# Performance work log

Measured on AMD Instinct MI355X. Metric: run time of the kernel, lower is better.

## Reference

```python
import jax, jax.numpy as jnp
import numpy as np

B, NQ, NKV = 4, 1024, 2048
DQ, DC, DI, H = 1024, 1024, 1024, 16
DH = DI // H
EPS = 1e-5


def layer_norm(x, gamma, beta):
    mu = jnp.mean(x, axis=-1, keepdims=True)
    var = jnp.var(x, axis=-1, keepdims=True)
    return (x - mu) * jax.lax.rsqrt(var + EPS) * gamma + beta


def setup_inputs() -> dict:
    key = jax.random.key(0)
    ks = jax.random.split(key, 6)
    s = 0.02
    return {
        "q": jax.random.normal(ks[0], (B, NQ, DQ), jnp.float32),
        "context": jax.random.normal(ks[1], (B, NKV, DC), jnp.float32),
        "Wq": jax.random.normal(ks[2], (DI, DQ), jnp.float32) * s,
        "Wkv": jax.random.normal(ks[3], (2 * DI, DC), jnp.float32) * s,
        "Wproj": jax.random.normal(ks[4], (DQ, DI), jnp.float32) * s,
        "bproj": jnp.zeros((DQ,), jnp.float32),
        "q_gamma": jnp.ones((DQ,), jnp.float32),
        "q_beta": jnp.zeros((DQ,), jnp.float32),
        "c_gamma": jnp.ones((DC,), jnp.float32),
        "c_beta": jnp.zeros((DC,), jnp.float32),
    }


def reference(q, context, Wq, Wkv, Wproj, bproj, q_gamma, q_beta, c_gamma, c_beta):
    scale = DH ** -0.5
    qn = layer_norm(q, q_gamma, q_beta)            # [b, nq, dq]
    cn = layer_norm(context, c_gamma, c_beta)      # [b, nkv, dc]
    qp = qn @ Wq.T                                  # [b, nq, di]
    kv = cn @ Wkv.T                                 # [b, nkv, 2*di]
    k, v = kv[..., :DI], kv[..., DI:]
    qh = qp.reshape(B, NQ, H, DH)
    kh = k.reshape(B, NKV, H, DH)
    vh = v.reshape(B, NKV, H, DH)
    attn = jnp.einsum('bnhd,bmhd->bhnm', qh, kh) * scale   # [b,h,nq,nkv]
    attn = jax.nn.softmax(attn, axis=-1)
    out = jnp.einsum('bhnm,bmhd->bnhd', attn, vh).reshape(B, NQ, DI)
    return out @ Wproj.T + bproj
```

## Files before the change

kernel.cpp:

```cpp
#include <hip/hip_runtime.h>
#include <hip/hip_bf16.h>
#include <stdint.h>

#define B_N 4
#define NQ 1024
#define NKV 2048
#define DI 1024
#define H 16
#define DH 64

using bf16 = __bf16;
typedef bf16 bf16x8 __attribute__((ext_vector_type(8)));
typedef bf16 bf16x4 __attribute__((ext_vector_type(4)));
typedef float f32x4 __attribute__((ext_vector_type(4)));

typedef const __attribute__((address_space(1))) void* gptr_t;
typedef __attribute__((address_space(3))) void* sptr_t;

__global__ __launch_bounds__(256) void cvt_all(const float* __restrict__ Wq,
    const float* __restrict__ Wkv, const float* __restrict__ Wproj,
    bf16* __restrict__ oq, bf16* __restrict__ okv, bf16* __restrict__ op) {
  int i = blockIdx.x * 256 + threadIdx.x;
  const float* src; bf16* dst; int j;
  if (i < 262144)      { src = Wq;    dst = oq;  j = i; }
  else if (i < 786432) { src = Wkv;   dst = okv; j = i - 262144; }
  else                 { src = Wproj; dst = op;  j = i - 786432; }
  float4 v = reinterpret_cast<const float4*>(src)[j];
  bf16x4 o;
  o[0] = (bf16)v.x; o[1] = (bf16)v.y; o[2] = (bf16)v.z; o[3] = (bf16)v.w;
  reinterpret_cast<bf16x4*>(dst)[j] = o;
}

__global__ __launch_bounds__(256) void ln_kernel(const float* __restrict__ q,
    const float* __restrict__ ctx,
    const float* __restrict__ qg, const float* __restrict__ qb,
    const float* __restrict__ cg, const float* __restrict__ cb,
    bf16* __restrict__ qn, bf16* __restrict__ cn) {
  int row = blockIdx.x;
  const float* x; const float* gamma; const float* beta; bf16* out; int r;
  if (row < 4096) { x = q;   gamma = qg; beta = qb; out = qn; r = row; }
  else            { x = ctx; gamma = cg; beta = cb; out = cn; r = row - 4096; }
  int t = threadIdx.x;
  const float4 v = reinterpret_cast<const float4*>(x + (size_t)r * 1024)[t];
  float s = v.x + v.y + v.z + v.w;
  float s2 = v.x*v.x + v.y*v.y + v.z*v.z + v.w*v.w;
#pragma unroll
  for (int m = 1; m < 64; m <<= 1) { s += __shfl_xor(s, m); s2 += __shfl_xor(s2, m); }
  __shared__ float red[8];
  int wid = t >> 6;
  if ((t & 63) == 0) { red[wid] = s; red[wid + 4] = s2; }
  __syncthreads();
  float ts  = red[0] + red[1] + red[2] + red[3];
  float ts2 = red[4] + red[5] + red[6] + red[7];
  float mean = ts * (1.0f / 1024.0f);
  float var  = ts2 * (1.0f / 1024.0f) - mean * mean;
  float rstd = rsqrtf(var + 1e-5f);
  float4 g  = reinterpret_cast<const float4*>(gamma)[t];
  float4 bb = reinterpret_cast<const float4*>(beta)[t];
  bf16x4 o;
  o[0] = (bf16)((v.x - mean) * rstd * g.x + bb.x);
  o[1] = (bf16)((v.y - mean) * rstd * g.y + bb.y);
  o[2] = (bf16)((v.z - mean) * rstd * g.z + bb.z);
  o[3] = (bf16)((v.w - mean) * rstd * g.w + bb.w);
  reinterpret_cast<bf16x4*>(out + (size_t)r * 1024)[t] = o;
}

template<int MODE, int BN>
__global__ __launch_bounds__(256) void gemm_bt(const bf16* __restrict__ A,
    const bf16* __restrict__ Bm, void* __restrict__ out0, void* __restrict__ out1,
    const float* __restrict__ bias, int M, int N) {
  constexpr int K = 1024;
  constexpr int MI = (BN == 128) ? 4 : 2;
  constexpr int NBL = (BN == 128) ? 4 : 2;
  __shared__ bf16 lA[128 * 64];
  __shared__ bf16 lB[BN * 64];
  const int cpx = gridDim.x >> 3;
  const int bid = (blockIdx.x & 7) * cpx + (blockIdx.x >> 3);
  const int nbn = N / BN;
  const int bm = bid / nbn, bn = bid - bm * nbn;
  const int m0 = bm << 7, n0 = bn * BN;
  const int tid = threadIdx.x;
  const int lane = tid & 63, wid = tid >> 6;
  const int rowb = (BN == 128) ? ((wid >> 1) * 64) : (wid * 32);
  const int colb = (BN == 128) ? ((wid & 1) * 64) : 0;
  const int l15 = lane & 15, lg = lane >> 4;

  f32x4 acc[MI][4] = {};

  const bf16* gA[4]; const bf16* gB[NBL];
#pragma unroll
  for (int u = 0; u < 4; ++u) {
    int s = tid + u * 256;
    int row = s >> 3, c8 = (s & 7) ^ (row & 7);
    gA[u] = A + (size_t)(m0 + row) * K + c8 * 8;
  }
#pragma unroll
  for (int u = 0; u < NBL; ++u) {
    int s = tid + u * 256;
    int row = s >> 3, c8 = (s & 7) ^ (row & 7);
    gB[u] = Bm + (size_t)(n0 + row) * K + c8 * 8;
  }

  const int sw = l15 & 7;

  for (int k0 = 0; k0 < K; k0 += 64) {
#pragma unroll
    for (int u = 0; u < 4; ++u)
      __builtin_amdgcn_global_load_lds((gptr_t)(gA[u] + k0), (sptr_t)(lA + (tid + u * 256) * 8), 16, 0, 0);
#pragma unroll
    for (int u = 0; u < NBL; ++u)
      __builtin_amdgcn_global_load_lds((gptr_t)(gB[u] + k0), (sptr_t)(lB + (tid + u * 256) * 8), 16, 0, 0);
    __syncthreads();
#pragma unroll
    for (int ks2 = 0; ks2 < 2; ++ks2) {
      const int soff = ((ks2 * 4 + lg) ^ sw) * 8;
      bf16x8 af[MI], bfr[4];
#pragma unroll
      for (int i = 0; i < MI; ++i)
        af[i]  = *reinterpret_cast<const bf16x8*>(lA + (rowb + i * 16 + l15) * 64 + soff);
#pragma unroll
      for (int j = 0; j < 4; ++j)
        bfr[j] = *reinterpret_cast<const bf16x8*>(lB + (colb + j * 16 + l15) * 64 + soff);
#pragma unroll
      for (int i = 0; i < MI; ++i)
#pragma unroll
        for (int j = 0; j < 4; ++j)
          acc[i][j] = __builtin_amdgcn_mfma_f32_16x16x32_bf16(af[i], bfr[j], acc[i][j], 0, 0, 0);
    }
    __syncthreads();
  }

  const int mB = m0 + rowb + lg * 4;
  const int nB = n0 + colb + l15;
  if constexpr (MODE == 0) {
    bf16* o = reinterpret_cast<bf16*>(out0);
    constexpr float SC = 0.125f * 1.44269504089f;
#pragma unroll
    for (int i = 0; i < MI; ++i)
#pragma unroll
      for (int j = 0; j < 4; ++j)
#pragma unroll
        for (int r = 0; r < 4; ++r)
          o[(size_t)(mB + i * 16 + r) * N + nB + j * 16] = (bf16)(acc[i][j][r] * SC);
  } else if constexpr (MODE == 2) {
    float* o = reinterpret_cast<float*>(out0);
#pragma unroll
    for (int j = 0; j < 4; ++j) {
      float bj = bias[nB + j * 16];
#pragma unroll
      for (int i = 0; i < MI; ++i)
#pragma unroll
        for (int r = 0; r < 4; ++r)
          o[(size_t)(mB + i * 16 + r) * N + nB + j * 16] = acc[i][j][r] + bj;
    }
  } else {
    if (n0 < 1024) {
      bf16* o = reinterpret_cast<bf16*>(out0);
#pragma unroll
      for (int i = 0; i < MI; ++i)
#pragma unroll
        for (int j = 0; j < 4; ++j)
#pragma unroll
          for (int r = 0; r < 4; ++r)
            o[(size_t)(mB + i * 16 + r) * 1024 + nB + j * 16] = (bf16)acc[i][j][r];
    } else {
      bf16* o = reinterpret_cast<bf16*>(out1);
#pragma unroll
      for (int i = 0; i < MI; ++i) {
        int m = mB + i * 16;
        int bb_ = m >> 11, kv = m & 2047;
        int u = kv & 63;
        int c = (u & 32) | ((u & 12) << 1) | ((u & 16) >> 2) | (u & 3);
        int col = (kv & ~63) | c;
#pragma unroll
        for (int j = 0; j < 4; ++j) {
          int nv = nB + j * 16 - 1024;
          bf16x4 pk;
          pk[0] = (bf16)acc[i][j][0]; pk[1] = (bf16)acc[i][j][1];
          pk[2] = (bf16)acc[i][j][2]; pk[3] = (bf16)acc[i][j][3];
          *reinterpret_cast<bf16x4*>(o + ((size_t)(bb_ << 10) + nv) * 2048 + col) = pk;
        }
      }
    }
  }
}

__global__ __launch_bounds__(512, 4) void attn_kernel(const bf16* __restrict__ qp,
    const bf16* __restrict__ kk, const bf16* __restrict__ vTp, bf16* __restrict__ out) {
  __shared__ bf16 smem[32768];
  const int pos = blockIdx.x;
  const int idx = pos >> 3;
  const int bh = ((idx >> 3) << 3) | (pos & 7);
  const int qt = idx & 7;
  const int b = bh >> 4, h = bh & 15;
  const int tid = threadIdx.x;
  const int lane = tid & 63, w = tid >> 6;
  const int l15 = lane & 15, lg = lane >> 4;

  const bf16* Qb = qp + (size_t)(b * NQ + qt * 128 + w * 16) * DI + h * DH;
  const bf16* Kb = kk + (size_t)b * NKV * DI + h * DH;
  const bf16* Vb = vTp + (size_t)(b * DI + h * DH) * NKV;

  const int sA = tid, sB = tid + 512;
  const int rKA = ((sA >> 7) << 4) | (sA & 15), cKA = ((sA >> 4) & 7) * 8;
  const int rKB = ((sB >> 7) << 4) | (sB & 15), cKB = ((sB >> 4) & 7) * 8;
  const int rVA = ((sA >> 8) << 4) | (sA & 15), cVA = ((sA >> 6) & 3) * 32 + ((sA >> 4) & 3) * 8;
  const int rVB = ((sB >> 8) << 4) | (sB & 15), cVB = ((sB >> 6) & 3) * 32 + ((sB >> 4) & 3) * 8;
  const bf16* pKA = Kb + (size_t)rKA * DI + cKA;
  const bf16* pKB = Kb + (size_t)rKB * DI + cKB;
  const bf16* pVA = Vb + (size_t)rVA * NKV + cVA;
  const bf16* pVB = Vb + (size_t)rVB * NKV + cVB;

#define STAGE_KV(bufsel, kv)                                                                        \
  do {                                                                                              \
    __builtin_amdgcn_global_load_lds((gptr_t)(pKA + (size_t)(kv) * DI),                             \
                                     (sptr_t)(smem + (bufsel) * 8192 + sA * 8), 16, 0, 0);          \
    __builtin_amdgcn_global_load_lds((gptr_t)(pKB + (size_t)(kv) * DI),                             \
                                     (sptr_t)(smem + (bufsel) * 8192 + sB * 8), 16, 0, 0);          \
    __builtin_amdgcn_global_load_lds((gptr_t)(pVA + (kv)),                                          \
                                     (sptr_t)(smem + 16384 + (bufsel) * 8192 + sA * 8), 16, 0, 0);  \
    __builtin_amdgcn_global_load_lds((gptr_t)(pVB + (kv)),                                          \
                                     (sptr_t)(smem + 16384 + (bufsel) * 8192 + sB * 8), 16, 0, 0);  \
  } while (0)

  bf16x8 qf[2];
#pragma unroll
  for (int ks = 0; ks < 2; ++ks)
    qf[ks] = *reinterpret_cast<const bf16x8*>(Qb + (size_t)l15 * DI + ks * 32 + lg * 8);

  f32x4 o[4] = {};
  float mrun = -1e30f;
  float lpart = 0.0f;

  STAGE_KV(0, 0);
  __syncthreads();
  int cur = 0;

  for (int kv0 = 0; kv0 < NKV; kv0 += 128) {
    const bool notlast = (kv0 + 128 < NKV);
    if (notlast) STAGE_KV(cur ^ 1, kv0 + 128);

    const bf16* Kl = smem + cur * 8192;
    const bf16* Vl = smem + 16384 + cur * 8192;

    f32x4 s[8] = {};
#pragma unroll
    for (int h2 = 0; h2 < 2; ++h2) {
      bf16x8 kf[4][2];
#pragma unroll
      for (int ni = 0; ni < 4; ++ni)
#pragma unroll
        for (int ks = 0; ks < 2; ++ks)
          kf[ni][ks] = *reinterpret_cast<const bf16x8*>(Kl + (((h2 * 4 + ni) * 2 + ks) * 64 + lane) * 8);
      __builtin_amdgcn_s_setprio(1);
#pragma unroll
      for (int ni = 0; ni < 4; ++ni)
#pragma unroll
        for (int ks = 0; ks < 2; ++ks)
          s[h2 * 4 + ni] = __builtin_amdgcn_mfma_f32_16x16x32_bf16(kf[ni][ks], qf[ks], s[h2 * 4 + ni], 0, 0, 0);
      __builtin_amdgcn_s_setprio(0);
    }

    f32x4 mv = s[0];
#pragma unroll
    for (int i = 1; i < 8; ++i) {
      mv[0] = fmaxf(mv[0], s[i][0]); mv[1] = fmaxf(mv[1], s[i][1]);
      mv[2] = fmaxf(mv[2], s[i][2]); mv[3] = fmaxf(mv[3], s[i][3]);
    }
    float pm = fmaxf(fmaxf(mv[0], mv[1]), fmaxf(mv[2], mv[3]));
    pm = fmaxf(pm, __shfl_xor(pm, 16));
    pm = fmaxf(pm, __shfl_xor(pm, 32));

    const bool noresc = __all(pm <= mrun);
    const float mnew = noresc ? mrun : fmaxf(mrun, pm);

    f32x4 sv = {};
#pragma unroll
    for (int i = 0; i < 8; ++i) {
#pragma unroll
      for (int r = 0; r < 4; ++r) {
        s[i][r] = __builtin_amdgcn_exp2f(s[i][r] - mnew);
        sv[r] += s[i][r];
      }
    }
    const float rs_local = (sv[0] + sv[1]) + (sv[2] + sv[3]);

    if (noresc) {
      lpart += rs_local;
    } else {
      float corr = __builtin_amdgcn_exp2f(mrun - mnew);
      lpart = lpart * corr + rs_local;
      mrun = mnew;
      float c0 = __shfl(corr, lg * 4 + 0);
      float c1 = __shfl(corr, lg * 4 + 1);
      float c2 = __shfl(corr, lg * 4 + 2);
      float c3 = __shfl(corr, lg * 4 + 3);
#pragma unroll
      for (int dt = 0; dt < 4; ++dt) {
        o[dt][0] *= c0; o[dt][1] *= c1; o[dt][2] *= c2; o[dt][3] *= c3;
      }
    }

    bf16x8 pa[4];
#pragma unroll
    for (int h2 = 0; h2 < 2; ++h2)
#pragma unroll
      for (int k2p = 0; k2p < 2; ++k2p)
#pragma unroll
        for (int jj = 0; jj < 4; ++jj) {
          pa[h2 * 2 + k2p][jj]     = (bf16)s[h2 * 4 + k2p * 2 + 0][jj];
          pa[h2 * 2 + k2p][4 + jj] = (bf16)s[h2 * 4 + k2p * 2 + 1][jj];
        }

    __builtin_amdgcn_s_setprio(1);
#pragma unroll
    for (int k2 = 0; k2 < 4; ++k2) {
      bf16x8 vf[4];
#pragma unroll
      for (int dt = 0; dt < 4; ++dt)
        vf[dt] = *reinterpret_cast<const bf16x8*>(Vl + ((dt * 4 + k2) * 64 + lane) * 8);
#pragma unroll
      for (int dt = 0; dt < 4; ++dt)
        o[dt] = __builtin_amdgcn_mfma_f32_16x16x32_bf16(pa[k2], vf[dt], o[dt], 0, 0, 0);
    }
    __builtin_amdgcn_s_setprio(0);

    if (notlast) __syncthreads();
    cur ^= 1;
  }
#undef STAGE_KV

  float lsum = lpart;
  lsum += __shfl_xor(lsum, 16);
  lsum += __shfl_xor(lsum, 32);
  const float inv = 1.0f / lsum;
  const float iv0 = __shfl(inv, lg * 4 + 0);
  const float iv1 = __shfl(inv, lg * 4 + 1);
  const float iv2 = __shfl(inv, lg * 4 + 2);
  const float iv3 = __shfl(inv, lg * 4 + 3);

  bf16* Ob = out + (size_t)(b * NQ + qt * 128 + w * 16) * DI + h * DH;
#pragma unroll
  for (int dt = 0; dt < 4; ++dt) {
    Ob[(size_t)(lg * 4 + 0) * DI + dt * 16 + l15] = (bf16)(o[dt][0] * iv0);
    Ob[(size_t)(lg * 4 + 1) * DI + dt * 16 + l15] = (bf16)(o[dt][1] * iv1);
    Ob[(size_t)(lg * 4 + 2) * DI + dt * 16 + l15] = (bf16)(o[dt][2] * iv2);
    Ob[(size_t)(lg * 4 + 3) * DI + dt * 16 + l15] = (bf16)(o[dt][3] * iv3);
  }
}

extern "C" void kernel_launch(void* const* d_in, const int* in_sizes, int n_in,
                              void* d_out, int out_size, void* d_ws, size_t ws_size,
                              hipStream_t stream) {
  const float* q     = (const float*)d_in[0];
  const float* ctx   = (const float*)d_in[1];
  const float* Wq    = (const float*)d_in[2];
  const float* Wkv   = (const float*)d_in[3];
  const float* Wproj = (const float*)d_in[4];
  const float* bproj = (const float*)d_in[5];
  const float* qg    = (const float*)d_in[6];
  const float* qb    = (const float*)d_in[7];
  const float* cg    = (const float*)d_in[8];
  const float* cb    = (const float*)d_in[9];

  char* ws = (char*)d_ws;
  bf16* qn    = (bf16*)(ws);
  bf16* cn    = (bf16*)(ws + ( 8ull << 20));
  bf16* Wq_b  = (bf16*)(ws + (24ull << 20));
  bf16* Wkv_b = (bf16*)(ws + (26ull << 20));
  bf16* Wp_b  = (bf16*)(ws + (30ull << 20));
  bf16* qpb   = (bf16*)(ws + (32ull << 20));
  bf16* kbuf  = (bf16*)(ws + (40ull << 20));
  bf16* vT    = (bf16*)(ws + (56ull << 20));
  bf16* aout  = (bf16*)(ws + (72ull << 20));

  cvt_all<<<4096, 256, 0, stream>>>(Wq, Wkv, Wproj, Wq_b, Wkv_b, Wp_b);
  ln_kernel<<<12288, 256, 0, stream>>>(q, ctx, qg, qb, cg, cb, qn, cn);

  gemm_bt<0, 64><<<512,  256, 0, stream>>>(qn,   Wq_b,  qpb,  nullptr, nullptr, 4096, 1024);
  gemm_bt<1,128><<<1024, 256, 0, stream>>>(cn,   Wkv_b, kbuf, vT,      nullptr, 8192, 2048);

  attn_kernel<<<512, 512, 0, stream>>>(qpb, kbuf, vT, aout);

  gemm_bt<2, 64><<<512,  256, 0, stream>>>(aout, Wp_b,  d_out, nullptr, bproj, 4096, 1024);
}
```

Before: 142.7 us.

## Merge Q and KV projection GEMMs into one launch; give attention waves two query tiles

The Q projection and KV projection GEMMs now run in a single launch, with block ranges dispatched to a shared gemm body. The Q GEMM also moves from 64-wide to 128-wide tiles. The attention kernel drops to 256 threads, and each wave now handles 32 query rows (two 16-row MFMA tiles), so every K/V fragment read from LDS is reused twice. This cuts launch overhead and tail effects and raises arithmetic intensity per LDS read, at the cost of more registers per wave and fewer waves per CU.

After: 165.5 us. 16.0% more time.

```diff
diff --git a/kernel.cpp b/kernel.cpp
--- a/kernel.cpp
+++ b/kernel.cpp
@@ -66,16 +66,13 @@
 }
 
 template<int MODE, int BN>
-__global__ __launch_bounds__(256) void gemm_bt(const bf16* __restrict__ A,
-    const bf16* __restrict__ Bm, void* __restrict__ out0, void* __restrict__ out1,
-    const float* __restrict__ bias, int M, int N) {
+__device__ __forceinline__ void gemm_body(bf16* lA, bf16* lB,
+    const bf16* __restrict__ A, const bf16* __restrict__ Bm,
+    void* __restrict__ out0, void* __restrict__ out1,
+    const float* __restrict__ bias, int M, int N, int bid) {
   constexpr int K = 1024;
   constexpr int MI = (BN == 128) ? 4 : 2;
   constexpr int NBL = (BN == 128) ? 4 : 2;
-  __shared__ bf16 lA[128 * 64];
-  __shared__ bf16 lB[BN * 64];
-  const int cpx = gridDim.x >> 3;
-  const int bid = (blockIdx.x & 7) * cpx + (blockIdx.x >> 3);
   const int nbn = N / BN;
   const int bm = bid / nbn, bn = bid - bm * nbn;
   const int m0 = bm << 7, n0 = bn * BN;
@@ -185,7 +182,35 @@
   }
 }
 
-__global__ __launch_bounds__(512, 4) void attn_kernel(const bf16* __restrict__ qp,
+template<int MODE, int BN>
+__global__ __launch_bounds__(256) void gemm_bt(const bf16* __restrict__ A,
+    const bf16* __restrict__ Bm, void* __restrict__ out0, void* __restrict__ out1,
+    const float* __restrict__ bias, int M, int N) {
+  __shared__ bf16 lA[128 * 64];
+  __shared__ bf16 lB[BN * 64];
+  const int cpx = gridDim.x >> 3;
+  const int bid = (blockIdx.x & 7) * cpx + (blockIdx.x >> 3);
+  gemm_body<MODE, BN>(lA, lB, A, Bm, out0, out1, bias, M, N, bid);
+}
+
+__global__ __launch_bounds__(256) void gemm_fused(
+    const bf16* __restrict__ qn, const bf16* __restrict__ Wq, void* __restrict__ qpb,
+    const bf16* __restrict__ cn, const bf16* __restrict__ Wkv,
+    void* __restrict__ kbuf, void* __restrict__ vT) {
+  __shared__ bf16 lA[128 * 64];
+  __shared__ bf16 lB[128 * 64];
+  if (blockIdx.x < 1024) {
+    int rb = blockIdx.x;
+    int bid = (rb & 7) * 128 + (rb >> 3);
+    gemm_body<1, 128>(lA, lB, cn, Wkv, kbuf, vT, nullptr, 8192, 2048, bid);
+  } else {
+    int rb = blockIdx.x - 1024;
+    int bid = (rb & 7) * 32 + (rb >> 3);
+    gemm_body<0, 128>(lA, lB, qn, Wq, qpb, nullptr, nullptr, 4096, 1024, bid);
+  }
+}
+
+__global__ __launch_bounds__(256) void attn_kernel(const bf16* __restrict__ qp,
     const bf16* __restrict__ kk, const bf16* __restrict__ vTp, bf16* __restrict__ out) {
   __shared__ bf16 smem[32768];
   const int pos = blockIdx.x;
@@ -197,53 +222,53 @@
   const int lane = tid & 63, w = tid >> 6;
   const int l15 = lane & 15, lg = lane >> 4;
 
-  const bf16* Qb = qp + (size_t)(b * NQ + qt * 128 + w * 16) * DI + h * DH;
+  const bf16* Qb = qp + (size_t)(b * NQ + qt * 128 + w * 32) * DI + h * DH;
   const bf16* Kb = kk + (size_t)b * NKV * DI + h * DH;
   const bf16* Vb = vTp + (size_t)(b * DI + h * DH) * NKV;
 
-  const int sA = tid, sB = tid + 512;
-  const int rKA = ((sA >> 7) << 4) | (sA & 15), cKA = ((sA >> 4) & 7) * 8;
-  const int rKB = ((sB >> 7) << 4) | (sB & 15), cKB = ((sB >> 4) & 7) * 8;
-  const int rVA = ((sA >> 8) << 4) | (sA & 15), cVA = ((sA >> 6) & 3) * 32 + ((sA >> 4) & 3) * 8;
-  const int rVB = ((sB >> 8) << 4) | (sB & 15), cVB = ((sB >> 6) & 3) * 32 + ((sB >> 4) & 3) * 8;
-  const bf16* pKA = Kb + (size_t)rKA * DI + cKA;
-  const bf16* pKB = Kb + (size_t)rKB * DI + cKB;
-  const bf16* pVA = Vb + (size_t)rVA * NKV + cVA;
-  const bf16* pVB = Vb + (size_t)rVB * NKV + cVB;
-
-#define STAGE_KV(bufsel, kv)                                                                        \
-  do {                                                                                              \
-    __builtin_amdgcn_global_load_lds((gptr_t)(pKA + (size_t)(kv) * DI),                             \
-                                     (sptr_t)(smem + (bufsel) * 8192 + sA * 8), 16, 0, 0);          \
-    __builtin_amdgcn_global_load_lds((gptr_t)(pKB + (size_t)(kv) * DI),                             \
-                                     (sptr_t)(smem + (bufsel) * 8192 + sB * 8), 16, 0, 0);          \
-    __builtin_amdgcn_global_load_lds((gptr_t)(pVA + (kv)),                                          \
-                                     (sptr_t)(smem + 16384 + (bufsel) * 8192 + sA * 8), 16, 0, 0);  \
-    __builtin_amdgcn_global_load_lds((gptr_t)(pVB + (kv)),                                          \
-                                     (sptr_t)(smem + 16384 + (bufsel) * 8192 + sB * 8), 16, 0, 0);  \
-  } while (0)
-
-  bf16x8 qf[2];
-#pragma unroll
-  for (int ks = 0; ks < 2; ++ks)
-    qf[ks] = *reinterpret_cast<const bf16x8*>(Qb + (size_t)l15 * DI + ks * 32 + lg * 8);
-
-  f32x4 o[4] = {};
+  const bf16* pK[4]; const bf16* pV[4];
+#pragma unroll
+  for (int u = 0; u < 4; ++u) {
+    int s = tid + u * 256;
+    int rK = ((s >> 7) << 4) | (s & 15), cK = ((s >> 4) & 7) * 8;
+    int rV = ((s >> 8) << 4) | (s & 15), cV = ((s >> 6) & 3) * 32 + ((s >> 4) & 3) * 8;
+    pK[u] = Kb + (size_t)rK * DI + cK;
+    pV[u] = Vb + (size_t)rV * NKV + cV;
+  }
+
+  auto STAGE = [&](int bufsel, int kv) {
+#pragma unroll
+    for (int u = 0; u < 4; ++u) {
+      __builtin_amdgcn_global_load_lds((gptr_t)(pK[u] + (size_t)kv * DI),
+          (sptr_t)(smem + bufsel * 8192 + (tid + u * 256) * 8), 16, 0, 0);
+      __builtin_amdgcn_global_load_lds((gptr_t)(pV[u] + kv),
+          (sptr_t)(smem + 16384 + bufsel * 8192 + (tid + u * 256) * 8), 16, 0, 0);
+    }
+  };
+
+  bf16x8 qf[2][2];
+#pragma unroll
+  for (int mi = 0; mi < 2; ++mi)
+#pragma unroll
+    for (int ks = 0; ks < 2; ++ks)
+      qf[mi][ks] = *reinterpret_cast<const bf16x8*>(Qb + (size_t)(mi * 16 + l15) * DI + ks * 32 + lg * 8);
+
+  f32x4 o[2][4] = {};
   float mrun = -1e30f;
-  float lpart = 0.0f;
-
-  STAGE_KV(0, 0);
+  float lpart0 = 0.0f, lpart1 = 0.0f;
+
+  STAGE(0, 0);
   __syncthreads();
   int cur = 0;
 
   for (int kv0 = 0; kv0 < NKV; kv0 += 128) {
     const bool notlast = (kv0 + 128 < NKV);
-    if (notlast) STAGE_KV(cur ^ 1, kv0 + 128);
+    if (notlast) STAGE(cur ^ 1, kv0 + 128);
 
     const bf16* Kl = smem + cur * 8192;
     const bf16* Vl = smem + 16384 + cur * 8192;
 
-    f32x4 s[8] = {};
+    f32x4 s[2][8] = {};
 #pragma unroll
     for (int h2 = 0; h2 < 2; ++h2) {
       bf16x8 kf[4][2];
@@ -254,18 +279,25 @@
           kf[ni][ks] = *reinterpret_cast<const bf16x8*>(Kl + (((h2 * 4 + ni) * 2 + ks) * 64 + lane) * 8);
       __builtin_amdgcn_s_setprio(1);
 #pragma unroll
-      for (int ni = 0; ni < 4; ++ni)
-#pragma unroll
-        for (int ks = 0; ks < 2; ++ks)
-          s[h2 * 4 + ni] = __builtin_amdgcn_mfma_f32_16x16x32_bf16(kf[ni][ks], qf[ks], s[h2 * 4 + ni], 0, 0, 0);
+      for (int mi = 0; mi < 2; ++mi)
+#pragma unroll
+        for (int ni = 0; ni < 4; ++ni)
+#pragma unroll
+          for (int ks = 0; ks < 2; ++ks)
+            s[mi][h2 * 4 + ni] = __builtin_amdgcn_mfma_f32_16x16x32_bf16(kf[ni][ks], qf[mi][ks], s[mi][h2 * 4 + ni], 0, 0, 0);
       __builtin_amdgcn_s_setprio(0);
     }
 
-    f32x4 mv = s[0];
+    f32x4 mv = s[0][0];
 #pragma unroll
     for (int i = 1; i < 8; ++i) {
-      mv[0] = fmaxf(mv[0], s[i][0]); mv[1] = fmaxf(mv[1], s[i][1]);
-      mv[2] = fmaxf(mv[2], s[i][2]); mv[3] = fmaxf(mv[3], s[i][3]);
+      mv[0] = fmaxf(mv[0], s[0][i][0]); mv[1] = fmaxf(mv[1], s[0][i][1]);
+      mv[2] = fmaxf(mv[2], s[0][i][2]); mv[3] = fmaxf(mv[3], s[0][i][3]);
+    }
+#pragma unroll
+    for (int i = 0; i < 8; ++i) {
+      mv[0] = fmaxf(mv[0], s[1][i][0]); mv[1] = fmaxf(mv[1], s[1][i][1]);
+      mv[2] = fmaxf(mv[2], s[1][i][2]); mv[3] = fmaxf(mv[3], s[1][i][3]);
     }
     float pm = fmaxf(fmaxf(mv[0], mv[1]), fmaxf(mv[2], mv[3]));
     pm = fmaxf(pm, __shfl_xor(pm, 16));
@@ -274,43 +306,61 @@
     const bool noresc = __all(pm <= mrun);
     const float mnew = noresc ? mrun : fmaxf(mrun, pm);
 
-    f32x4 sv = {};
-#pragma unroll
-    for (int i = 0; i < 8; ++i) {
-#pragma unroll
-      for (int r = 0; r < 4; ++r) {
-        s[i][r] = __builtin_amdgcn_exp2f(s[i][r] - mnew);
-        sv[r] += s[i][r];
-      }
-    }
-    const float rs_local = (sv[0] + sv[1]) + (sv[2] + sv[3]);
+    float rs0, rs1;
+    {
+      f32x4 sv = {};
+#pragma unroll
+      for (int i = 0; i < 8; ++i)
+#pragma unroll
+        for (int r = 0; r < 4; ++r) {
+          s[0][i][r] = __builtin_amdgcn_exp2f(s[0][i][r] - mnew);
+          sv[r] += s[0][i][r];
+        }
+      rs0 = (sv[0] + sv[1]) + (sv[2] + sv[3]);
+    }
+    {
+      f32x4 sv = {};
+#pragma unroll
+      for (int i = 0; i < 8; ++i)
+#pragma unroll
+        for (int r = 0; r < 4; ++r) {
+          s[1][i][r] = __builtin_amdgcn_exp2f(s[1][i][r] - mnew);
+          sv[r] += s[1][i][r];
+        }
+      rs1 = (sv[0] + sv[1]) + (sv[2] + sv[3]);
+    }
 
     if (noresc) {
-      lpart += rs_local;
+      lpart0 += rs0; lpart1 += rs1;
     } else {
       float corr = __builtin_amdgcn_exp2f(mrun - mnew);
-      lpart = lpart * corr + rs_local;
+      lpart0 = lpart0 * corr + rs0;
+      lpart1 = lpart1 * corr + rs1;
       mrun = mnew;
       float c0 = __shfl(corr, lg * 4 + 0);
       float c1 = __shfl(corr, lg * 4 + 1);
       float c2 = __shfl(corr, lg * 4 + 2);
       float c3 = __shfl(corr, lg * 4 + 3);
 #pragma unroll
-      for (int dt = 0; dt < 4; ++dt) {
-        o[dt][0] *= c0; o[dt][1] *= c1; o[dt][2] *= c2; o[dt][3] *= c3;
-      }
-    }
-
-    bf16x8 pa[4];
-#pragma unroll
-    for (int h2 = 0; h2 < 2; ++h2)
-#pragma unroll
-      for (int k2p = 0; k2p < 2; ++k2p)
-#pragma unroll
-        for (int jj = 0; jj < 4; ++jj) {
-          pa[h2 * 2 + k2p][jj]     = (bf16)s[h2 * 4 + k2p * 2 + 0][jj];
-          pa[h2 * 2 + k2p][4 + jj] = (bf16)s[h2 * 4 + k2p * 2 + 1][jj];
+      for (int mi = 0; mi < 2; ++mi)
+#pragma unroll
+        for (int dt = 0; dt < 4; ++dt) {
+          o[mi][dt][0] *= c0; o[mi][dt][1] *= c1; o[mi][dt][2] *= c2; o[mi][dt][3] *= c3;
         }
+    }
+
+    bf16x8 pa[2][4];
+#pragma unroll
+    for (int mi = 0; mi < 2; ++mi)
+#pragma unroll
+      for (int h2 = 0; h2 < 2; ++h2)
+#pragma unroll
+        for (int k2p = 0; k2p < 2; ++k2p)
+#pragma unroll
+          for (int jj = 0; jj < 4; ++jj) {
+            pa[mi][h2 * 2 + k2p][jj]     = (bf16)s[mi][h2 * 4 + k2p * 2 + 0][jj];
+            pa[mi][h2 * 2 + k2p][4 + jj] = (bf16)s[mi][h2 * 4 + k2p * 2 + 1][jj];
+          }
 
     __builtin_amdgcn_s_setprio(1);
 #pragma unroll
@@ -320,32 +370,35 @@
       for (int dt = 0; dt < 4; ++dt)
         vf[dt] = *reinterpret_cast<const bf16x8*>(Vl + ((dt * 4 + k2) * 64 + lane) * 8);
 #pragma unroll
-      for (int dt = 0; dt < 4; ++dt)
-        o[dt] = __builtin_amdgcn_mfma_f32_16x16x32_bf16(pa[k2], vf[dt], o[dt], 0, 0, 0);
+      for (int mi = 0; mi < 2; ++mi)
+#pragma unroll
+        for (int dt = 0; dt < 4; ++dt)
+          o[mi][dt] = __builtin_amdgcn_mfma_f32_16x16x32_bf16(pa[mi][k2], vf[dt], o[mi][dt], 0, 0, 0);
     }
     __builtin_amdgcn_s_setprio(0);
 
     if (notlast) __syncthreads();
     cur ^= 1;
   }
-#undef STAGE_KV
-
-  float lsum = lpart;
-  lsum += __shfl_xor(lsum, 16);
-  lsum += __shfl_xor(lsum, 32);
-  const float inv = 1.0f / lsum;
-  const float iv0 = __shfl(inv, lg * 4 + 0);
-  const float iv1 = __shfl(inv, lg * 4 + 1);
-  const float iv2 = __shfl(inv, lg * 4 + 2);
-  const float iv3 = __shfl(inv, lg * 4 + 3);
-
-  bf16* Ob = out + (size_t)(b * NQ + qt * 128 + w * 16) * DI + h * DH;
-#pragma unroll
-  for (int dt = 0; dt < 4; ++dt) {
-    Ob[(size_t)(lg * 4 + 0) * DI + dt * 16 + l15] = (bf16)(o[dt][0] * iv0);
-    Ob[(size_t)(lg * 4 + 1) * DI + dt * 16 + l15] = (bf16)(o[dt][1] * iv1);
-    Ob[(size_t)(lg * 4 + 2) * DI + dt * 16 + l15] = (bf16)(o[dt][2] * iv2);
-    Ob[(size_t)(lg * 4 + 3) * DI + dt * 16 + l15] = (bf16)(o[dt][3] * iv3);
+
+#pragma unroll
+  for (int mi = 0; mi < 2; ++mi) {
+    float lsum = (mi == 0) ? lpart0 : lpart1;
+    lsum += __shfl_xor(lsum, 16);
+    lsum += __shfl_xor(lsum, 32);
+    const float inv = 1.0f / lsum;
+    const float iv0 = __shfl(inv, lg * 4 + 0);
+    const float iv1 = __shfl(inv, lg * 4 + 1);
+    const float iv2 = __shfl(inv, lg * 4 + 2);
+    const float iv3 = __shfl(inv, lg * 4 + 3);
+    bf16* Ob = out + (size_t)(b * NQ + qt * 128 + w * 32 + mi * 16) * DI + h * DH;
+#pragma unroll
+    for (int dt = 0; dt < 4; ++dt) {
+      Ob[(size_t)(lg * 4 + 0) * DI + dt * 16 + l15] = (bf16)(o[mi][dt][0] * iv0);
+      Ob[(size_t)(lg * 4 + 1) * DI + dt * 16 + l15] = (bf16)(o[mi][dt][1] * iv1);
+      Ob[(size_t)(lg * 4 + 2) * DI + dt * 16 + l15] = (bf16)(o[mi][dt][2] * iv2);
+      Ob[(size_t)(lg * 4 + 3) * DI + dt * 16 + l15] = (bf16)(o[mi][dt][3] * iv3);
+    }
   }
 }
 
@@ -377,10 +430,9 @@
   cvt_all<<<4096, 256, 0, stream>>>(Wq, Wkv, Wproj, Wq_b, Wkv_b, Wp_b);
   ln_kernel<<<12288, 256, 0, stream>>>(q, ctx, qg, qb, cg, cb, qn, cn);
 
-  gemm_bt<0, 64><<<512,  256, 0, stream>>>(qn,   Wq_b,  qpb,  nullptr, nullptr, 4096, 1024);
-  gemm_bt<1,128><<<1024, 256, 0, stream>>>(cn,   Wkv_b, kbuf, vT,      nullptr, 8192, 2048);
-
-  attn_kernel<<<512, 512, 0, stream>>>(qpb, kbuf, vT, aout);
-
-  gemm_bt<2, 64><<<512,  256, 0, stream>>>(aout, Wp_b,  d_out, nullptr, bproj, 4096, 1024);
-}
+  gemm_fused<<<1280, 256, 0, stream>>>(qn, Wq_b, qpb, cn, Wkv_b, kbuf, vT);
+
+  attn_kernel<<<512, 256, 0, stream>>>(qpb, kbuf, vT, aout);
+
+  gemm_bt<2, 64><<<512, 256, 0, stream>>>(aout, Wp_b, d_out, nullptr, bproj, 4096, 1024);
+}
```

## Fuse Q and KV projection GEMMs into a 3-stage pipelined 256x128 kernel

Applied to the files above, without the earlier changes.

The separate Q and KV projection GEMM launches become one 640-block launch that dispatches on block index. Each block now computes a 256x128 tile with 512 threads and a K-step of 32. A triple-buffered global_load_lds pipeline with explicit vmcnt waits overlaps loads with MFMA work, and setprio raises wave priority during the MFMA section. This aims to hide global-load latency and cut launch and tail overhead. In exchange it uses about 72KB of LDS per block, which limits occupancy, and drops the XOR swizzle on the LDS layout, which may add bank conflicts. The output projection GEMM is split out unchanged as its own kernel.

New measurement: 151.7 us, median of 3. 6.3% more time.

```diff
diff --git a/kernel.cpp b/kernel.cpp
--- a/kernel.cpp
+++ b/kernel.cpp
@@ -65,70 +65,73 @@
   reinterpret_cast<bf16x4*>(out + (size_t)r * 1024)[t] = o;
 }
 
-template<int MODE, int BN>
-__global__ __launch_bounds__(256) void gemm_bt(const bf16* __restrict__ A,
-    const bf16* __restrict__ Bm, void* __restrict__ out0, void* __restrict__ out1,
-    const float* __restrict__ bias, int M, int N) {
+template<int MODE>
+__device__ __forceinline__ void gemm_pipe_body(bf16* lA, bf16* lB,
+    const bf16* __restrict__ A, const bf16* __restrict__ Bm,
+    void* __restrict__ out0, void* __restrict__ out1, int N, int bid) {
   constexpr int K = 1024;
-  constexpr int MI = (BN == 128) ? 4 : 2;
-  constexpr int NBL = (BN == 128) ? 4 : 2;
-  __shared__ bf16 lA[128 * 64];
-  __shared__ bf16 lB[BN * 64];
-  const int cpx = gridDim.x >> 3;
-  const int bid = (blockIdx.x & 7) * cpx + (blockIdx.x >> 3);
-  const int nbn = N / BN;
+  const int nbn = N >> 7;
   const int bm = bid / nbn, bn = bid - bm * nbn;
-  const int m0 = bm << 7, n0 = bn * BN;
+  const int m0 = bm << 8, n0 = bn << 7;
   const int tid = threadIdx.x;
   const int lane = tid & 63, wid = tid >> 6;
-  const int rowb = (BN == 128) ? ((wid >> 1) * 64) : (wid * 32);
-  const int colb = (BN == 128) ? ((wid & 1) * 64) : 0;
+  const int wr = wid >> 1, wc = wid & 1;
+  const int rowb = wr * 64, colb = wc * 64;
   const int l15 = lane & 15, lg = lane >> 4;
 
-  f32x4 acc[MI][4] = {};
-
-  const bf16* gA[4]; const bf16* gB[NBL];
-#pragma unroll
-  for (int u = 0; u < 4; ++u) {
-    int s = tid + u * 256;
-    int row = s >> 3, c8 = (s & 7) ^ (row & 7);
-    gA[u] = A + (size_t)(m0 + row) * K + c8 * 8;
-  }
-#pragma unroll
-  for (int u = 0; u < NBL; ++u) {
-    int s = tid + u * 256;
-    int row = s >> 3, c8 = (s & 7) ^ (row & 7);
-    gB[u] = Bm + (size_t)(n0 + row) * K + c8 * 8;
-  }
-
-  const int sw = l15 & 7;
-
-  for (int k0 = 0; k0 < K; k0 += 64) {
-#pragma unroll
-    for (int u = 0; u < 4; ++u)
-      __builtin_amdgcn_global_load_lds((gptr_t)(gA[u] + k0), (sptr_t)(lA + (tid + u * 256) * 8), 16, 0, 0);
-#pragma unroll
-    for (int u = 0; u < NBL; ++u)
-      __builtin_amdgcn_global_load_lds((gptr_t)(gB[u] + k0), (sptr_t)(lB + (tid + u * 256) * 8), 16, 0, 0);
-    __syncthreads();
-#pragma unroll
-    for (int ks2 = 0; ks2 < 2; ++ks2) {
-      const int soff = ((ks2 * 4 + lg) ^ sw) * 8;
-      bf16x8 af[MI], bfr[4];
-#pragma unroll
-      for (int i = 0; i < MI; ++i)
-        af[i]  = *reinterpret_cast<const bf16x8*>(lA + (rowb + i * 16 + l15) * 64 + soff);
+  f32x4 acc[4][4] = {};
+
+  const int sA1 = tid + 512;
+  const bf16* gA0 = A  + (size_t)(m0 + (tid >> 2)) * K + ((tid & 3) << 3);
+  const bf16* gA1 = A  + (size_t)(m0 + (sA1 >> 2)) * K + ((sA1 & 3) << 3);
+  const bf16* gB0 = Bm + (size_t)(n0 + (tid >> 2)) * K + ((tid & 3) << 3);
+
+#define PSTAGE(buf, k0)                                                                              \
+  do {                                                                                               \
+    __builtin_amdgcn_global_load_lds((gptr_t)(gA0 + (k0)),                                           \
+        (sptr_t)(lA + (buf) * 8192 + tid * 8), 16, 0, 0);                                            \
+    __builtin_amdgcn_global_load_lds((gptr_t)(gA1 + (k0)),                                           \
+        (sptr_t)(lA + (buf) * 8192 + sA1 * 8), 16, 0, 0);                                            \
+    __builtin_amdgcn_global_load_lds((gptr_t)(gB0 + (k0)),                                           \
+        (sptr_t)(lB + (buf) * 4096 + tid * 8), 16, 0, 0);                                            \
+  } while (0)
+
+  PSTAGE(0, 0);
+  PSTAGE(1, 32);
+  int cur = 0;
+
+  for (int kt = 0; kt < 32; ++kt) {
+    int nxt = cur + 2; if (nxt >= 3) nxt -= 3;
+    if (kt < 30) {
+      PSTAGE(nxt, (kt + 2) * 32);
+      asm volatile("s_waitcnt vmcnt(6)" ::: "memory");
+    } else if (kt == 30) {
+      asm volatile("s_waitcnt vmcnt(3)" ::: "memory");
+    } else {
+      asm volatile("s_waitcnt vmcnt(0)" ::: "memory");
+    }
+    __builtin_amdgcn_s_barrier();
+
+    const bf16* lAc = lA + cur * 8192;
+    const bf16* lBc = lB + cur * 4096;
+    bf16x8 af[4], bfr[4];
+#pragma unroll
+    for (int i = 0; i < 4; ++i)
+      af[i]  = *reinterpret_cast<const bf16x8*>(lAc + (rowb + i * 16 + l15) * 32 + lg * 8);
+#pragma unroll
+    for (int j = 0; j < 4; ++j)
+      bfr[j] = *reinterpret_cast<const bf16x8*>(lBc + (colb + j * 16 + l15) * 32 + lg * 8);
+    __builtin_amdgcn_s_setprio(1);
+#pragma unroll
+    for (int i = 0; i < 4; ++i)
 #pragma unroll
       for (int j = 0; j < 4; ++j)
-        bfr[j] = *reinterpret_cast<const bf16x8*>(lB + (colb + j * 16 + l15) * 64 + soff);
-#pragma unroll
-      for (int i = 0; i < MI; ++i)
-#pragma unroll
-        for (int j = 0; j < 4; ++j)
-          acc[i][j] = __builtin_amdgcn_mfma_f32_16x16x32_bf16(af[i], bfr[j], acc[i][j], 0, 0, 0);
-    }
-    __syncthreads();
-  }
+        acc[i][j] = __builtin_amdgcn_mfma_f32_16x16x32_bf16(af[i], bfr[j], acc[i][j], 0, 0, 0);
+    __builtin_amdgcn_s_setprio(0);
+    __builtin_amdgcn_s_barrier();
+    cur = (cur == 2) ? 0 : cur + 1;
+  }
+#undef PSTAGE
 
   const int mB = m0 + rowb + lg * 4;
   const int nB = n0 + colb + l15;
@@ -136,28 +139,17 @@
     bf16* o = reinterpret_cast<bf16*>(out0);
     constexpr float SC = 0.125f * 1.44269504089f;
 #pragma unroll
-    for (int i = 0; i < MI; ++i)
+    for (int i = 0; i < 4; ++i)
 #pragma unroll
       for (int j = 0; j < 4; ++j)
 #pragma unroll
         for (int r = 0; r < 4; ++r)
           o[(size_t)(mB + i * 16 + r) * N + nB + j * 16] = (bf16)(acc[i][j][r] * SC);
-  } else if constexpr (MODE == 2) {
-    float* o = reinterpret_cast<float*>(out0);
-#pragma unroll
-    for (int j = 0; j < 4; ++j) {
-      float bj = bias[nB + j * 16];
-#pragma unroll
-      for (int i = 0; i < MI; ++i)
-#pragma unroll
-        for (int r = 0; r < 4; ++r)
-          o[(size_t)(mB + i * 16 + r) * N + nB + j * 16] = acc[i][j][r] + bj;
-    }
   } else {
     if (n0 < 1024) {
       bf16* o = reinterpret_cast<bf16*>(out0);
 #pragma unroll
-      for (int i = 0; i < MI; ++i)
+      for (int i = 0; i < 4; ++i)
 #pragma unroll
         for (int j = 0; j < 4; ++j)
 #pragma unroll
@@ -166,7 +158,7 @@
     } else {
       bf16* o = reinterpret_cast<bf16*>(out1);
 #pragma unroll
-      for (int i = 0; i < MI; ++i) {
+      for (int i = 0; i < 4; ++i) {
         int m = mB + i * 16;
         int bb_ = m >> 11, kv = m & 2047;
         int u = kv & 63;
@@ -182,6 +174,96 @@
         }
       }
     }
+  }
+}
+
+__global__ __launch_bounds__(512, 4) void gemm_fused(
+    const bf16* __restrict__ qn, const bf16* __restrict__ Wq, void* __restrict__ qpb,
+    const bf16* __restrict__ cn, const bf16* __restrict__ Wkv,
+    void* __restrict__ kbuf, void* __restrict__ vT) {
+  __shared__ bf16 lA[3 * 8192];
+  __shared__ bf16 lB[3 * 4096];
+  if (blockIdx.x < 512) {
+    int rb = blockIdx.x;
+    int bid = (rb & 7) * 64 + (rb >> 3);
+    gemm_pipe_body<1>(lA, lB, cn, Wkv, kbuf, vT, 2048, bid);
+  } else {
+    int rb = blockIdx.x - 512;
+    int bid = (rb & 7) * 16 + (rb >> 3);
+    gemm_pipe_body<0>(lA, lB, qn, Wq, qpb, nullptr, 1024, bid);
+  }
+}
+
+__global__ __launch_bounds__(256) void gemm_proj(const bf16* __restrict__ A,
+    const bf16* __restrict__ Bm, float* __restrict__ out0,
+    const float* __restrict__ bias, int M, int N) {
+  constexpr int K = 1024;
+  __shared__ bf16 lA[128 * 64];
+  __shared__ bf16 lB[64 * 64];
+  const int cpx = gridDim.x >> 3;
+  const int bid = (blockIdx.x & 7) * cpx + (blockIdx.x >> 3);
+  const int nbn = N >> 6;
+  const int bm = bid / nbn, bn = bid - bm * nbn;
+  const int m0 = bm << 7, n0 = bn << 6;
+  const int tid = threadIdx.x;
+  const int lane = tid & 63, wid = tid >> 6;
+  const int rowb = wid * 32;
+  const int l15 = lane & 15, lg = lane >> 4;
+
+  f32x4 acc[2][4] = {};
+
+  const bf16* gA[4]; const bf16* gB[2];
+#pragma unroll
+  for (int u = 0; u < 4; ++u) {
+    int s = tid + u * 256;
+    int row = s >> 3, c8 = (s & 7) ^ (row & 7);
+    gA[u] = A + (size_t)(m0 + row) * K + c8 * 8;
+  }
+#pragma unroll
+  for (int u = 0; u < 2; ++u) {
+    int s = tid + u * 256;
+    int row = s >> 3, c8 = (s & 7) ^ (row & 7);
+    gB[u] = Bm + (size_t)(n0 + row) * K + c8 * 8;
+  }
+  const int sw = l15 & 7;
+
+  for (int k0 = 0; k0 < K; k0 += 64) {
+#pragma unroll
+    for (int u = 0; u < 4; ++u)
+      __builtin_amdgcn_global_load_lds((gptr_t)(gA[u] + k0), (sptr_t)(lA + (tid + u * 256) * 8), 16, 0, 0);
+#pragma unroll
+    for (int u = 0; u < 2; ++u)
+      __builtin_amdgcn_global_load_lds((gptr_t)(gB[u] + k0), (sptr_t)(lB + (tid + u * 256) * 8), 16, 0, 0);
+    __syncthreads();
+#pragma unroll
+    for (int ks2 = 0; ks2 < 2; ++ks2) {
+      const int soff = ((ks2 * 4 + lg) ^ sw) * 8;
+      bf16x8 af[2], bfr[4];
+#pragma unroll
+      for (int i = 0; i < 2; ++i)
+        af[i]  = *reinterpret_cast<const bf16x8*>(lA + (rowb + i * 16 + l15) * 64 + soff);
+#pragma unroll
+      for (int j = 0; j < 4; ++j)
+        bfr[j] = *reinterpret_cast<const bf16x8*>(lB + (j * 16 + l15) * 64 + soff);
+#pragma unroll
+      for (int i = 0; i < 2; ++i)
+#pragma unroll
+        for (int j = 0; j < 4; ++j)
+          acc[i][j] = __builtin_amdgcn_mfma_f32_16x16x32_bf16(af[i], bfr[j], acc[i][j], 0, 0, 0);
+    }
+    __syncthreads();
+  }
+
+  const int mB = m0 + rowb + lg * 4;
+  const int nB = n0 + l15;
+#pragma unroll
+  for (int j = 0; j < 4; ++j) {
+    float bj = bias[nB + j * 16];
+#pragma unroll
+    for (int i = 0; i < 2; ++i)
+#pragma unroll
+      for (int r = 0; r < 4; ++r)
+        out0[(size_t)(mB + i * 16 + r) * N + nB + j * 16] = acc[i][j][r] + bj;
   }
 }
 
@@ -377,10 +459,9 @@
   cvt_all<<<4096, 256, 0, stream>>>(Wq, Wkv, Wproj, Wq_b, Wkv_b, Wp_b);
   ln_kernel<<<12288, 256, 0, stream>>>(q, ctx, qg, qb, cg, cb, qn, cn);
 
-  gemm_bt<0, 64><<<512,  256, 0, stream>>>(qn,   Wq_b,  qpb,  nullptr, nullptr, 4096, 1024);
-  gemm_bt<1,128><<<1024, 256, 0, stream>>>(cn,   Wkv_b, kbuf, vT,      nullptr, 8192, 2048);
+  gemm_fused<<<640, 512, 0, stream>>>(qn, Wq_b, qpb, cn, Wkv_b, kbuf, vT);
 
   attn_kernel<<<512, 512, 0, stream>>>(qpb, kbuf, vT, aout);
 
-  gemm_bt<2, 64><<<512,  256, 0, stream>>>(aout, Wp_b,  d_out, nullptr, bproj, 4096, 1024);
-}
+  gemm_proj<<<512, 256, 0, stream>>>(aout, Wp_b, (float*)d_out, bproj, 4096, 1024);
+}
```
